# Optimization experiments

Measured on AMD Instinct MI355X. Metric: run time of the kernel, lower is better.

The kernel has to match this reference:

```python
import jax, jax.numpy as jnp
import numpy as np

GROUPS = 32
EPS = 1e-5


def setup_inputs() -> dict:
    key = jax.random.key(0)
    ks = jax.random.split(key, 8)
    B, C, H, W = 4, 512, 64, 64
    s = 1.0 / np.sqrt(C)  # conv1x1 fan-in init scale
    return {
        "x": jax.random.normal(ks[0], (B, C, H, W), dtype=jnp.float32),
        "gn_gamma": jnp.ones((C,), dtype=jnp.float32),
        "gn_beta": jnp.zeros((C,), dtype=jnp.float32),
        "wq": jax.random.normal(ks[1], (C, C), dtype=jnp.float32) * s,
        "bq": jnp.zeros((C,), dtype=jnp.float32),
        "wk": jax.random.normal(ks[2], (C, C), dtype=jnp.float32) * s,
        "bk": jnp.zeros((C,), dtype=jnp.float32),
        "wv": jax.random.normal(ks[3], (C, C), dtype=jnp.float32) * s,
        "bv": jnp.zeros((C,), dtype=jnp.float32),
    }


def reference(x, gn_gamma, gn_beta, wq, bq, wk, bk, wv, bv):
    B, C, H, W = x.shape
    N = H * W
    # GroupNorm over (channels-within-group, H, W)
    xg = x.reshape(B, GROUPS, C // GROUPS, H, W)
    mean = xg.mean(axis=(2, 3, 4), keepdims=True)
    var = xg.var(axis=(2, 3, 4), keepdims=True)
    xn = ((xg - mean) * jax.lax.rsqrt(var + EPS)).reshape(B, C, H, W)
    xn = xn * gn_gamma[None, :, None, None] + gn_beta[None, :, None, None]
    # 1x1 convs as channel matmuls over flattened spatial tokens: (B, C, N)
    xf = xn.reshape(B, C, N)
    q = jnp.einsum("oc,bcn->bon", wq, xf) + bq[None, :, None]  # (B, Co, N)
    k = jnp.einsum("oc,bcn->bon", wk, xf) + bk[None, :, None]
    v = jnp.einsum("oc,bcn->bon", wv, xf) + bv[None, :, None]
    # scores[b, m, n] = <Q_m, K_n> / sqrt(Co); full N x N matrix as in original
    scale = 1.0 / jnp.sqrt(jnp.asarray(C, dtype=x.dtype))
    scores = jnp.einsum("bcm,bcn->bmn", q, k) * scale  # (B, N, N)
    prob = jax.nn.softmax(scores, axis=-1)
    # out[b, c, m] = sum_n prob[b, m, n] * v[b, c, n]
    attn = jnp.einsum("bmn,bcn->bcm", prob, v).reshape(B, C, H, W)
    return x + attn  # ResLine is Identity since ch_in == ch_out
```

## Files before the change

### kernel.cpp

```cpp
#include <hip/hip_runtime.h>
#include <cstdint>

typedef __attribute__((ext_vector_type(8))) short short8;
typedef __attribute__((ext_vector_type(4))) float floatx4;
typedef __attribute__((ext_vector_type(8))) int intx8;

__device__ __forceinline__ unsigned short f2bf(float f) {
  unsigned int u = __float_as_uint(f);
  u += 0x7fffu + ((u >> 16) & 1u);
  return (unsigned short)(u >> 16);
}

__global__ __launch_bounds__(256) void gn_partial_kernel(
    const float* __restrict__ x, float* __restrict__ gsums) {
  const int b = blockIdx.x >> 8;
  const int g = (blockIdx.x >> 3) & 31;
  const int e = blockIdx.x & 7;
  const long long off = ((long long)(b * 512 + g * 16)) * 4096;
  const float4* xp = (const float4*)(x + off) + e * 2048;
  float s = 0.f, ss = 0.f;
  for (int i = threadIdx.x; i < 2048; i += 256) {
    float4 v = xp[i];
    s  += v.x + v.y + v.z + v.w;
    ss += v.x * v.x + v.y * v.y + v.z * v.z + v.w * v.w;
  }
  for (int off2 = 32; off2; off2 >>= 1) { s += __shfl_down(s, off2); ss += __shfl_down(ss, off2); }
  __shared__ float sb[8];
  const int lane = threadIdx.x & 63, wave = threadIdx.x >> 6;
  if (lane == 0) { sb[wave] = s; sb[4 + wave] = ss; }
  __syncthreads();
  if (threadIdx.x == 0) {
    atomicAdd(gsums + (b * 32 + g) * 2,     sb[0] + sb[1] + sb[2] + sb[3]);
    atomicAdd(gsums + (b * 32 + g) * 2 + 1, sb[4] + sb[5] + sb[6] + sb[7]);
  }
}

__global__ __launch_bounds__(256) void gn_finalize_kernel(
    const float* __restrict__ gsums, const float* __restrict__ gamma,
    const float* __restrict__ beta, float* __restrict__ scale,
    float* __restrict__ shift) {
  const int i = blockIdx.x * 256 + threadIdx.x;
  const int b = i >> 9;
  const int c = i & 511;
  const int g = c >> 4;
  const float S  = gsums[(b * 32 + g) * 2];
  const float SS = gsums[(b * 32 + g) * 2 + 1];
  const float mean = S * (1.f / 65536.f);
  const float var  = SS * (1.f / 65536.f) - mean * mean;
  const float inv  = rsqrtf(var + 1e-5f);
  const float sc = gamma[c] * inv;
  scale[i] = sc;
  shift[i] = beta[c] - mean * sc;
}

__global__ __launch_bounds__(256) void wcvt_zero_kernel(
    const float* __restrict__ wq, const float* __restrict__ wk,
    const float* __restrict__ wv, unsigned short* __restrict__ w16,
    float* __restrict__ zp, int nzero) {
  const int gi = blockIdx.x * 256 + threadIdx.x;
  if (gi < 196608) {
    const int m = gi >> 16;
    const int i = gi & 65535;
    const float* src = (m == 0) ? wq : (m == 1) ? wk : wv;
    float4 v = *((const float4*)src + i);
    ushort4 o;
    o.x = f2bf(v.x); o.y = f2bf(v.y); o.z = f2bf(v.z); o.w = f2bf(v.w);
    *((ushort4*)(w16 + (long long)m * 262144) + i) = o;
  } else {
    const int zi = gi - 196608;
    if (zi < nzero) zp[zi] = 0.f;
  }
}

__global__ __launch_bounds__(256) void norm_transpose_kernel(
    const float* __restrict__ x, const float* __restrict__ scale,
    const float* __restrict__ shift, unsigned short* __restrict__ xnt) {
  const int b = blockIdx.z;
  const int n0 = blockIdx.x * 64;
  const int c0 = blockIdx.y * 64;
  const int t = threadIdx.x;
  __shared__ unsigned short tile[64][65];
  {
    const int cl = t >> 2;
    const int nc = (t & 3) * 16;
    const int c = c0 + cl;
    const float* xp = x + ((long long)b * 512 + c) * 4096 + n0 + nc;
    const float sc = scale[b * 512 + c];
    const float sh = shift[b * 512 + c];
#pragma unroll
    for (int j = 0; j < 16; j += 4) {
      float4 v = *(const float4*)(xp + j);
      tile[cl][nc + j + 0] = f2bf(v.x * sc + sh);
      tile[cl][nc + j + 1] = f2bf(v.y * sc + sh);
      tile[cl][nc + j + 2] = f2bf(v.z * sc + sh);
      tile[cl][nc + j + 3] = f2bf(v.w * sc + sh);
    }
  }
  __syncthreads();
  {
    const int nl = t >> 2;
    const int cc = (t & 3) * 16;
    union { unsigned short u[16]; uint4 q[2]; } o;
#pragma unroll
    for (int j = 0; j < 16; ++j) o.u[j] = tile[cc + j][nl];
    unsigned short* op = xnt + ((long long)b * 4096 + n0 + nl) * 512 + c0 + cc;
    *((uint4*)op) = o.q[0];
    *((uint4*)op + 1) = o.q[1];
  }
}

__global__ __launch_bounds__(256) void zero_kernel(float* __restrict__ p, int n) {
  const int i = blockIdx.x * 256 + threadIdx.x;
  if (i < n) p[i] = 0.f;
}

template <int EPI>
__global__ __launch_bounds__(256) void gemm_tn_kernel(
    const unsigned short* __restrict__ A, const unsigned short* __restrict__ B,
    void* __restrict__ C, const float* __restrict__ bias,
    const float* __restrict__ bias2,
    int lda, int ldb, int ldc, int K,
    long long sA, long long sB, long long sC) {
  const int tid = threadIdx.x;
  const int lane = tid & 63;
  const int wave = tid >> 6;
  const int m0 = blockIdx.x * 128;
  const int n0 = blockIdx.y * 128;
  const int bz = blockIdx.z;
  A += (long long)bz * sA;
  B += (long long)bz * sB;

  __shared__ unsigned short smem[17408];
  unsigned short* As = smem;
  unsigned short* Bs = smem + 8192;

  floatx4 acc[4][4];
#pragma unroll
  for (int i = 0; i < 4; ++i)
#pragma unroll
    for (int j = 0; j < 4; ++j) acc[i][j] = (floatx4){0.f, 0.f, 0.f, 0.f};

  const unsigned short* ag[4];
  const unsigned short* bg[4];
  unsigned ldsoff[4];
#pragma unroll
  for (int i = 0; i < 4; ++i) {
    const int idx = i * 256 + tid;
    const int r = idx >> 3;
    const int g = idx & 7;
    const int gs = g ^ (r & 7);
    ag[i] = A + (long long)(m0 + r) * lda + gs * 8;
    bg[i] = B + (long long)(n0 + r) * ldb + gs * 8;
    ldsoff[i] = (unsigned)(i * 256 + wave * 64) * 8;
  }

  const int l15 = lane & 15;
  const int wm = (wave >> 1) * 64;
  const int wn = (wave & 1) * 64;

  for (int k0 = 0; k0 < K; k0 += 64) {
#pragma unroll
    for (int i = 0; i < 4; ++i) {
      __builtin_amdgcn_global_load_lds(
          (const __attribute__((address_space(1))) void*)(ag[i] + k0),
          (__attribute__((address_space(3))) void*)(As + ldsoff[i]), 16, 0, 0);
      __builtin_amdgcn_global_load_lds(
          (const __attribute__((address_space(1))) void*)(bg[i] + k0),
          (__attribute__((address_space(3))) void*)(Bs + ldsoff[i]), 16, 0, 0);
    }
    __syncthreads();
#pragma unroll
    for (int kk = 0; kk < 64; kk += 32) {
      const int gq = (kk >> 3) + (lane >> 4);
      short8 af[4], bfr[4];
#pragma unroll
      for (int mt = 0; mt < 4; ++mt) {
        const int row = wm + mt * 16 + l15;
        af[mt] = *(const short8*)&As[row * 64 + ((gq ^ (row & 7)) << 3)];
      }
#pragma unroll
      for (int nt = 0; nt < 4; ++nt) {
        const int row = wn + nt * 16 + l15;
        bfr[nt] = *(const short8*)&Bs[row * 64 + ((gq ^ (row & 7)) << 3)];
      }
#pragma unroll
      for (int mt = 0; mt < 4; ++mt)
#pragma unroll
        for (int nt = 0; nt < 4; ++nt)
          acc[mt][nt] = __builtin_amdgcn_mfma_f32_16x16x32_bf16(
              af[mt], bfr[nt], acc[mt][nt], 0, 0, 0);
    }
    __syncthreads();
  }

  const int r0 = (lane >> 4) * 4;

  if (EPI == 6) {
    unsigned char* t8 = (unsigned char*)smem;
    const float* bp = (m0 >= 512) ? bias2 : bias;
    const int mb = m0 & 511;
#pragma unroll
    for (int mt = 0; mt < 4; ++mt) {
      const int ml = wm + mt * 16 + r0;
      const float b0 = bp[mb + ml], b1 = bp[mb + ml + 1];
      const float b2 = bp[mb + ml + 2], b3 = bp[mb + ml + 3];
      const int gw = ml >> 4;
      const int mby = ml & 15;
#pragma unroll
      for (int nt = 0; nt < 4; ++nt) {
        const int nl = wn + nt * 16 + l15;
        int p = __builtin_amdgcn_cvt_pk_fp8_f32(acc[mt][nt][0] + b0,
                                                acc[mt][nt][1] + b1, 0, false);
        p = __builtin_amdgcn_cvt_pk_fp8_f32(acc[mt][nt][2] + b2,
                                            acc[mt][nt][3] + b3, p, true);
        *(int*)&t8[nl * 128 + ((gw ^ (nl & 7)) << 4) + mby] = p;
      }
    }
    __syncthreads();
    unsigned char* o8 = (unsigned char*)C + (long long)bz * sC;
#pragma unroll
    for (int t = 0; t < 4; ++t) {
      const int gid = t * 256 + tid;
      const int row = gid >> 3;
      const int gc = gid & 7;
      uint4 v = *(const uint4*)&t8[row * 128 + ((gc ^ (row & 7)) << 4)];
      *(uint4*)&o8[(long long)(n0 + row) * ldc + m0 + gc * 16] = v;
    }
    return;
  }

  if (EPI == 3) {
    unsigned char* t8 = (unsigned char*)smem;
#pragma unroll
    for (int mt = 0; mt < 4; ++mt) {
      const int ml = wm + mt * 16 + r0;
      const float b0 = bias[m0 + ml],     b1 = bias[m0 + ml + 1];
      const float b2 = bias[m0 + ml + 2], b3 = bias[m0 + ml + 3];
#pragma unroll
      for (int nt = 0; nt < 4; ++nt) {
        const int nl = wn + nt * 16 + l15;
        int p0 = __builtin_amdgcn_cvt_pk_fp8_f32(acc[mt][nt][0] + b0,
                                                 acc[mt][nt][1] + b1, 0, false);
        int p1 = __builtin_amdgcn_cvt_pk_fp8_f32(acc[mt][nt][2] + b2,
                                                 acc[mt][nt][3] + b3, 0, false);
        t8[(ml + 0) * 144 + nl] = (unsigned char)(p0 & 0xff);
        t8[(ml + 1) * 144 + nl] = (unsigned char)((p0 >> 8) & 0xff);
        t8[(ml + 2) * 144 + nl] = (unsigned char)(p1 & 0xff);
        t8[(ml + 3) * 144 + nl] = (unsigned char)((p1 >> 8) & 0xff);
      }
    }
    __syncthreads();
    unsigned char* o8 = (unsigned char*)C + (long long)bz * sC;
#pragma unroll
    for (int t = 0; t < 4; ++t) {
      const int gid = t * 256 + tid;
      const int row = gid >> 3;
      const int gc = gid & 7;
      uint4 v = *(const uint4*)&t8[row * 144 + gc * 16];
      *(uint4*)&o8[(long long)(m0 + row) * ldc + n0 + gc * 16] = v;
    }
    return;
  }

#pragma unroll
  for (int mt = 0; mt < 4; ++mt) {
#pragma unroll
    for (int nt = 0; nt < 4; ++nt) {
      const int nl = wn + nt * 16 + l15;
#pragma unroll
      for (int r = 0; r < 4; ++r) {
        const int ml = wm + mt * 16 + r0 + r;
        smem[ml * 136 + nl] = f2bf(acc[mt][nt][r] + bias[m0 + ml]);
      }
    }
  }
  __syncthreads();
  {
    unsigned short* o = (unsigned short*)C + (long long)bz * sC;
#pragma unroll
    for (int j = 0; j < 8; ++j) {
      const int gid = j * 256 + tid;
      const int m = gid >> 4;
      const int gc = gid & 15;
      short8 v = *(const short8*)&smem[m * 136 + gc * 8];
      *(short8*)&o[(long long)(m0 + m) * ldc + n0 + gc * 8] = v;
    }
  }
}

__global__ __launch_bounds__(256) void sgemm_fp8_kernel(
    const unsigned char* __restrict__ A, const unsigned char* __restrict__ B,
    unsigned char* __restrict__ S, float* __restrict__ lsum,
    long long sA, long long sB, long long sC, long long sL) {
  const int tid = threadIdx.x;
  const int lane = tid & 63;
  const int wave = tid >> 6;
  const int quad = lane >> 4;
  const int l15 = lane & 15;
  const int j0 = blockIdx.x * 128;
  const int i0 = blockIdx.y * 128;
  const int bz = blockIdx.z;
  A += (long long)bz * sA;
  B += (long long)bz * sB;

  __shared__ unsigned short smem[17408];
  unsigned char* As = (unsigned char*)smem;
  unsigned char* Bs = (unsigned char*)smem + 16384;

  floatx4 acc[4][4];
#pragma unroll
  for (int i = 0; i < 4; ++i)
#pragma unroll
    for (int j = 0; j < 4; ++j) acc[i][j] = (floatx4){0.f, 0.f, 0.f, 0.f};

  const unsigned char* ag[4];
  const unsigned char* bg[4];
  unsigned ldsoff[4];
#pragma unroll
  for (int i = 0; i < 4; ++i) {
    const int idx = i * 256 + tid;
    const int r = idx >> 3;
    const int g = idx & 7;
    const int gs = g ^ (r & 7);
    ag[i] = A + (long long)(j0 + r) * 1024 + gs * 16;
    bg[i] = B + (long long)(i0 + r) * 1024 + gs * 16;
    ldsoff[i] = (unsigned)(i * 256 + wave * 64) * 16;
  }

  const int wj = (wave >> 1) * 64;
  const int wi = (wave & 1) * 64;

  for (int k0 = 0; k0 < 512; k0 += 128) {
#pragma unroll
    for (int i = 0; i < 4; ++i) {
      __builtin_amdgcn_global_load_lds(
          (const __attribute__((address_space(1))) void*)(ag[i] + k0),
          (__attribute__((address_space(3))) void*)(As + ldsoff[i]), 16, 0, 0);
      __builtin_amdgcn_global_load_lds(
          (const __attribute__((address_space(1))) void*)(bg[i] + k0),
          (__attribute__((address_space(3))) void*)(Bs + ldsoff[i]), 16, 0, 0);
    }
    __syncthreads();
    intx8 af[4], bq[4];
#pragma unroll
    for (int t = 0; t < 4; ++t) {
      {
        const int row = wj + t * 16 + l15;
        const int r7 = row & 7;
        const uint4 x0 = *(const uint4*)(As + row * 128 + (((2 * quad) ^ r7) << 4));
        const uint4 x1 = *(const uint4*)(As + row * 128 + (((2 * quad + 1) ^ r7) << 4));
        af[t] = (intx8){(int)x0.x, (int)x0.y, (int)x0.z, (int)x0.w,
                        (int)x1.x, (int)x1.y, (int)x1.z, (int)x1.w};
      }
      {
        const int row = wi + t * 16 + l15;
        const int r7 = row & 7;
        const uint4 x0 = *(const uint4*)(Bs + row * 128 + (((2 * quad) ^ r7) << 4));
        const uint4 x1 = *(const uint4*)(Bs + row * 128 + (((2 * quad + 1) ^ r7) << 4));
        bq[t] = (intx8){(int)x0.x, (int)x0.y, (int)x0.z, (int)x0.w,
                        (int)x1.x, (int)x1.y, (int)x1.z, (int)x1.w};
      }
    }
#pragma unroll
    for (int jt = 0; jt < 4; ++jt)
#pragma unroll
      for (int it = 0; it < 4; ++it)
        acc[jt][it] = __builtin_amdgcn_mfma_scale_f32_16x16x128_f8f6f4(
            af[jt], bq[it], acc[jt][it], 0, 0, 0, 127, 0, 127);
    __syncthreads();
  }

  const float SCL = 0.044194173824159216f;
  const int jr = quad * 4;
  unsigned char* t8 = (unsigned char*)smem;
  float rs_it[4] = {0.f, 0.f, 0.f, 0.f};
#pragma unroll
  for (int jt = 0; jt < 4; ++jt) {
#pragma unroll
    for (int it = 0; it < 4; ++it) {
      const int il = wi + it * 16 + l15;
      const int jl = wj + jt * 16 + jr;
      const float e0 = __expf(acc[jt][it][0] * SCL);
      const float e1 = __expf(acc[jt][it][1] * SCL);
      const float e2 = __expf(acc[jt][it][2] * SCL);
      const float e3 = __expf(acc[jt][it][3] * SCL);
      rs_it[it] += e0 + e1 + e2 + e3;
      int p = __builtin_amdgcn_cvt_pk_fp8_f32(e0, e1, 0, false);
      p = __builtin_amdgcn_cvt_pk_fp8_f32(e2, e3, p, true);
      *(int*)&t8[il * 144 + jl] = p;
    }
  }
  float* lrow = lsum + (long long)bz * sL;
#pragma unroll
  for (int it = 0; it < 4; ++it) {
    float rs = rs_it[it];
    rs += __shfl_xor(rs, 16);
    rs += __shfl_xor(rs, 32);
    if (quad == 0) atomicAdd(lrow + i0 + wi + it * 16 + l15, rs);
  }
  __syncthreads();
  unsigned char* o = S + (long long)bz * sC;
#pragma unroll
  for (int t = 0; t < 4; ++t) {
    const int gid = t * 256 + tid;
    const int row = gid >> 3;
    const int gc = gid & 7;
    uint4 v = *(const uint4*)&t8[row * 144 + gc * 16];
    *(uint4*)&o[(long long)(i0 + row) * 4096 + j0 + gc * 16] = v;
  }
}

__global__ __launch_bounds__(512, 2) void pv_kernel(
    const unsigned char* __restrict__ A,
    const unsigned char* __restrict__ B,
    float* __restrict__ out, const float* __restrict__ res,
    const float* __restrict__ lsum,
    long long sA, long long sB, long long sC, long long sL) {
  const int id = blockIdx.x;
  const int xcd = id & 7;
  const int slot = id >> 3;
  const int m0 = (slot & 3) * 128;
  const int grp = xcd + 8 * (slot >> 2);
  const int n0 = (grp & 15) * 256;
  const int bz = grp >> 4;
  A += (long long)bz * sA;
  B += (long long)bz * sB;

  const int tid = threadIdx.x;
  const int lane = tid & 63;
  const int wave = tid >> 6;
  const int l15 = lane & 15;
  const int quad = lane >> 4;
  const int wm = (wave >> 2) * 64;
  const int wn = (wave & 3) * 64;

  __shared__ unsigned char smem[147456];

  floatx4 acc[4][4];
#pragma unroll
  for (int i = 0; i < 4; ++i)
#pragma unroll
    for (int j = 0; j < 4; ++j) acc[i][j] = (floatx4){0.f, 0.f, 0.f, 0.f};

  const unsigned char* ag[2];
  const unsigned char* bg[4];
  unsigned ao[2], bo[4];
#pragma unroll
  for (int j = 0; j < 2; ++j) {
    const int idx = j * 512 + tid;
    const int r = idx >> 3;
    const int g = idx & 7;
    ag[j] = A + (long long)(m0 + r) * 4096 + ((g ^ (r & 7)) << 4);
    ao[j] = (unsigned)(j * 512 + wave * 64) * 16;
  }
#pragma unroll
  for (int j = 0; j < 4; ++j) {
    const int idx = j * 512 + tid;
    const int r = idx >> 3;
    const int g = idx & 7;
    bg[j] = B + (long long)(n0 + r) * 4096 + ((g ^ (r & 7)) << 4);
    bo[j] = 16384u + (unsigned)(j * 512 + wave * 64) * 16;
  }

#define PV_GLDS(gp, lp)                                              \
  __builtin_amdgcn_global_load_lds(                                  \
      (const __attribute__((address_space(1))) void*)(gp),           \
      (__attribute__((address_space(3))) void*)(lp), 16, 0, 0)
#define PV_STAGE(tt, base)                                           \
  {                                                                  \
    PV_GLDS(ag[0] + (tt) * 128, smem + (base) + ao[0]);              \
    PV_GLDS(ag[1] + (tt) * 128, smem + (base) + ao[1]);              \
    PV_GLDS(bg[0] + (tt) * 128, smem + (base) + bo[0]);              \
    PV_GLDS(bg[1] + (tt) * 128, smem + (base) + bo[1]);              \
    PV_GLDS(bg[2] + (tt) * 128, smem + (base) + bo[2]);              \
    PV_GLDS(bg[3] + (tt) * 128, smem + (base) + bo[3]);              \
  }

  PV_STAGE(0, 0);
  PV_STAGE(1, 49152);
  asm volatile("s_waitcnt vmcnt(6)" ::: "memory");
  __builtin_amdgcn_s_barrier();

  int cur = 0;
  for (int t = 0; t < 32; ++t) {
    const unsigned char* As = smem + cur * 49152;
    const unsigned char* Bs = As + 16384;
    const int nb = (cur == 0) ? 2 : cur - 1;
    const int nbase = nb * 49152;
    const bool st = (t < 30);

    intx8 af[4], bq[4];
#pragma unroll
    for (int tt = 0; tt < 4; ++tt) {
      {
        const int row = wm + tt * 16 + l15;
        const int r7 = row & 7;
        const uint4 x0 = *(const uint4*)(As + row * 128 + (((2 * quad) ^ r7) << 4));
        const uint4 x1 = *(const uint4*)(As + row * 128 + (((2 * quad + 1) ^ r7) << 4));
        af[tt] = (intx8){(int)x0.x, (int)x0.y, (int)x0.z, (int)x0.w,
                         (int)x1.x, (int)x1.y, (int)x1.z, (int)x1.w};
      }
      {
        const int row = wn + tt * 16 + l15;
        const int r7 = row & 7;
        const uint4 x0 = *(const uint4*)(Bs + row * 128 + (((2 * quad) ^ r7) << 4));
        const uint4 x1 = *(const uint4*)(Bs + row * 128 + (((2 * quad + 1) ^ r7) << 4));
        bq[tt] = (intx8){(int)x0.x, (int)x0.y, (int)x0.z, (int)x0.w,
                         (int)x1.x, (int)x1.y, (int)x1.z, (int)x1.w};
      }
    }
    __builtin_amdgcn_sched_barrier(0);
    if (st) PV_STAGE(t + 2, nbase);
    asm volatile("s_waitcnt lgkmcnt(0)" ::: "memory");
    __builtin_amdgcn_sched_barrier(0);
    __builtin_amdgcn_s_setprio(1);
#pragma unroll
    for (int mt = 0; mt < 4; ++mt)
#pragma unroll
      for (int nt = 0; nt < 4; ++nt)
        acc[mt][nt] = __builtin_amdgcn_mfma_scale_f32_16x16x128_f8f6f4(
            af[mt], bq[nt], acc[mt][nt], 0, 0, 0, 127, 0, 127);
    __builtin_amdgcn_s_setprio(0);
    if (st) {
      asm volatile("s_waitcnt vmcnt(6)" ::: "memory");
    } else {
      asm volatile("s_waitcnt vmcnt(0)" ::: "memory");
    }
    __builtin_amdgcn_s_barrier();

    cur = (cur == 2) ? 0 : cur + 1;
  }
#undef PV_GLDS
#undef PV_STAGE

  const int r0 = (lane >> 4) * 4;
  float* o = out + (long long)bz * sC;
  const float* rr = res + (long long)bz * sC;
  const float* lrow = lsum + (long long)bz * sL;
  float inv[4];
#pragma unroll
  for (int nt = 0; nt < 4; ++nt) inv[nt] = 1.f / lrow[n0 + wn + nt * 16 + l15];
#pragma unroll
  for (int mt = 0; mt < 4; ++mt) {
#pragma unroll
    for (int nt = 0; nt < 4; ++nt) {
      const int n = n0 + wn + nt * 16 + l15;
#pragma unroll
      for (int r = 0; r < 4; ++r) {
        const int m = m0 + wm + mt * 16 + r0 + r;
        const long long off = (long long)m * 4096 + n;
        o[off] = acc[mt][nt][r] * inv[nt] + rr[off];
      }
    }
  }
}

extern "C" void kernel_launch(void* const* d_in, const int* in_sizes, int n_in,
                              void* d_out, int out_size, void* d_ws, size_t ws_size,
                              hipStream_t stream) {
  const float* x     = (const float*)d_in[0];
  const float* gamma = (const float*)d_in[1];
  const float* beta  = (const float*)d_in[2];
  const float* wq    = (const float*)d_in[3];
  const float* bq    = (const float*)d_in[4];
  const float* wk    = (const float*)d_in[5];
  const float* bk    = (const float*)d_in[6];
  const float* wv    = (const float*)d_in[7];
  const float* bv    = (const float*)d_in[8];
  float* out = (float*)d_out;

  const long long sTok = 4096LL * 512;
  const long long sQK8 = 4096LL * 1024;
  const long long sS8  = 4096LL * 4096;
  const long long sV8  = 512LL * 4096;

  char* ws = (char*)d_ws;
  float* scale = (float*)ws;
  float* shift = (float*)(ws + 8192);
  unsigned short* w16 = (unsigned short*)(ws + 16384);
  unsigned short* xnt = (unsigned short*)(ws + 1589248);
  unsigned char*  qk8 = (unsigned char*)(ws + 18366464);
  unsigned char*  vv8 = (unsigned char*)(ws + 51920896);

  const bool full = ws_size >= 202982400ULL;

  float* lsum;
  int nzero;
  if (full) {
    lsum = (float*)(ws + 202915840);
    nzero = 16384 + 256;
  } else {
    lsum = (float*)(ws + 102252544);
    nzero = 4096 + 256;
  }
  float* gsums = lsum + nzero - 256;

  wcvt_zero_kernel<<<768 + (nzero + 255) / 256, 256, 0, stream>>>(
      wq, wk, wv, w16, lsum, nzero);
  gn_partial_kernel<<<1024, 256, 0, stream>>>(x, gsums);
  gn_finalize_kernel<<<8, 256, 0, stream>>>(gsums, gamma, beta, scale, shift);
  norm_transpose_kernel<<<dim3(64, 8, 4), 256, 0, stream>>>(x, scale, shift, xnt);

  gemm_tn_kernel<6><<<dim3(8, 32, 4), 256, 0, stream>>>(
      w16, xnt, qk8, bq, bk, 512, 512, 1024, 512, 0, sTok, sQK8);
  gemm_tn_kernel<3><<<dim3(4, 32, 4), 256, 0, stream>>>(
      w16 + 524288, xnt, vv8, bv, nullptr, 512, 512, 4096, 512, 0, sTok, sV8);

  if (full) {
    unsigned char* S8 = (unsigned char*)(ws + 68698112);
    sgemm_fp8_kernel<<<dim3(32, 32, 4), 256, 0, stream>>>(
        qk8 + 512, qk8, S8, lsum, sQK8, sQK8, sS8, 4096);
    pv_kernel<<<256, 512, 0, stream>>>(
        vv8, S8, out, x, lsum, sV8, sS8, sTok, 4096);
  } else {
    unsigned char* S8 = (unsigned char*)(ws + 68698112);
    for (int b = 0; b < 4; ++b) {
      if (b) zero_kernel<<<16, 256, 0, stream>>>(lsum, 4096);
      sgemm_fp8_kernel<<<dim3(32, 32, 1), 256, 0, stream>>>(
          qk8 + (long long)b * sQK8 + 512, qk8 + (long long)b * sQK8, S8, lsum,
          0, 0, 0, 0);
      pv_kernel<<<64, 512, 0, stream>>>(
          vv8 + (long long)b * sV8, S8, out + (long long)b * sTok,
          x + (long long)b * sTok, lsum, 0, 0, 0, 0);
    }
  }
}
```

Before: 242.9 us.

## Enlarge QK score tile and triple-buffer fp8 loads into LDS

The fp8 score GEMM now uses 512-thread blocks computing 128x256 tiles, with eight waves in a 2x4 layout. Staging is three-deep: two stages are prefetched up front, and each iteration issues the next async global-to-LDS load before its MFMAs. Explicit vmcnt/lgkmcnt waits and raw barriers replace the two __syncthreads per K step, and MFMA issue is raised in priority. The goal is to hide global load latency and reuse each A tile across more columns. The cost is 144 KB of LDS per block, which limits occupancy to one block per CU.

New measurement: 246.5 us. No clear change (+1.5%).

```diff
diff --git a/kernel.cpp b/kernel.cpp
--- a/kernel.cpp
+++ b/kernel.cpp
@@ -288,24 +288,26 @@
   }
 }
 
-__global__ __launch_bounds__(256) void sgemm_fp8_kernel(
-    const unsigned char* __restrict__ A, const unsigned char* __restrict__ B,
+__global__ __launch_bounds__(512, 2) void sgemm_fp8_kernel(
+    const unsigned char* __restrict__ A,
+    const unsigned char* __restrict__ B,
     unsigned char* __restrict__ S, float* __restrict__ lsum,
     long long sA, long long sB, long long sC, long long sL) {
+  const int j0 = blockIdx.x * 128;
+  const int i0 = blockIdx.y * 256;
+  const int bz = blockIdx.z;
+  A += (long long)bz * sA;
+  B += (long long)bz * sB;
+
   const int tid = threadIdx.x;
   const int lane = tid & 63;
   const int wave = tid >> 6;
+  const int l15 = lane & 15;
   const int quad = lane >> 4;
-  const int l15 = lane & 15;
-  const int j0 = blockIdx.x * 128;
-  const int i0 = blockIdx.y * 128;
-  const int bz = blockIdx.z;
-  A += (long long)bz * sA;
-  B += (long long)bz * sB;
-
-  __shared__ unsigned short smem[17408];
-  unsigned char* As = (unsigned char*)smem;
-  unsigned char* Bs = (unsigned char*)smem + 16384;
+  const int wm = (wave >> 2) * 64;
+  const int wn = (wave & 3) * 64;
+
+  __shared__ unsigned char smem[147456];
 
   floatx4 acc[4][4];
 #pragma unroll
@@ -313,78 +315,111 @@
 #pragma unroll
     for (int j = 0; j < 4; ++j) acc[i][j] = (floatx4){0.f, 0.f, 0.f, 0.f};
 
-  const unsigned char* ag[4];
+  const unsigned char* ag[2];
   const unsigned char* bg[4];
-  unsigned ldsoff[4];
-#pragma unroll
-  for (int i = 0; i < 4; ++i) {
-    const int idx = i * 256 + tid;
+  unsigned ao[2], bo[4];
+#pragma unroll
+  for (int j = 0; j < 2; ++j) {
+    const int idx = j * 512 + tid;
     const int r = idx >> 3;
     const int g = idx & 7;
-    const int gs = g ^ (r & 7);
-    ag[i] = A + (long long)(j0 + r) * 1024 + gs * 16;
-    bg[i] = B + (long long)(i0 + r) * 1024 + gs * 16;
-    ldsoff[i] = (unsigned)(i * 256 + wave * 64) * 16;
-  }
-
-  const int wj = (wave >> 1) * 64;
-  const int wi = (wave & 1) * 64;
-
-  for (int k0 = 0; k0 < 512; k0 += 128) {
-#pragma unroll
-    for (int i = 0; i < 4; ++i) {
-      __builtin_amdgcn_global_load_lds(
-          (const __attribute__((address_space(1))) void*)(ag[i] + k0),
-          (__attribute__((address_space(3))) void*)(As + ldsoff[i]), 16, 0, 0);
-      __builtin_amdgcn_global_load_lds(
-          (const __attribute__((address_space(1))) void*)(bg[i] + k0),
-          (__attribute__((address_space(3))) void*)(Bs + ldsoff[i]), 16, 0, 0);
-    }
-    __syncthreads();
+    ag[j] = A + (long long)(j0 + r) * 1024 + ((g ^ (r & 7)) << 4);
+    ao[j] = (unsigned)(j * 512 + wave * 64) * 16;
+  }
+#pragma unroll
+  for (int j = 0; j < 4; ++j) {
+    const int idx = j * 512 + tid;
+    const int r = idx >> 3;
+    const int g = idx & 7;
+    bg[j] = B + (long long)(i0 + r) * 1024 + ((g ^ (r & 7)) << 4);
+    bo[j] = 16384u + (unsigned)(j * 512 + wave * 64) * 16;
+  }
+
+#define SG_GLDS(gp, lp)                                              \
+  __builtin_amdgcn_global_load_lds(                                  \
+      (const __attribute__((address_space(1))) void*)(gp),           \
+      (__attribute__((address_space(3))) void*)(lp), 16, 0, 0)
+#define SG_STAGE(tt, base)                                           \
+  {                                                                  \
+    SG_GLDS(ag[0] + (tt) * 128, smem + (base) + ao[0]);              \
+    SG_GLDS(ag[1] + (tt) * 128, smem + (base) + ao[1]);              \
+    SG_GLDS(bg[0] + (tt) * 128, smem + (base) + bo[0]);              \
+    SG_GLDS(bg[1] + (tt) * 128, smem + (base) + bo[1]);              \
+    SG_GLDS(bg[2] + (tt) * 128, smem + (base) + bo[2]);              \
+    SG_GLDS(bg[3] + (tt) * 128, smem + (base) + bo[3]);              \
+  }
+
+  SG_STAGE(0, 0);
+  SG_STAGE(1, 49152);
+  asm volatile("s_waitcnt vmcnt(6)" ::: "memory");
+  __builtin_amdgcn_s_barrier();
+
+  int cur = 0;
+  for (int t = 0; t < 4; ++t) {
+    const unsigned char* As = smem + cur * 49152;
+    const unsigned char* Bs = As + 16384;
+    const int nb = (cur == 0) ? 2 : cur - 1;
+    const int nbase = nb * 49152;
+    const bool st = (t < 2);
+
     intx8 af[4], bq[4];
 #pragma unroll
-    for (int t = 0; t < 4; ++t) {
+    for (int tt = 0; tt < 4; ++tt) {
       {
-        const int row = wj + t * 16 + l15;
+        const int row = wm + tt * 16 + l15;
         const int r7 = row & 7;
         const uint4 x0 = *(const uint4*)(As + row * 128 + (((2 * quad) ^ r7) << 4));
         const uint4 x1 = *(const uint4*)(As + row * 128 + (((2 * quad + 1) ^ r7) << 4));
-        af[t] = (intx8){(int)x0.x, (int)x0.y, (int)x0.z, (int)x0.w,
-                        (int)x1.x, (int)x1.y, (int)x1.z, (int)x1.w};
+        af[tt] = (intx8){(int)x0.x, (int)x0.y, (int)x0.z, (int)x0.w,
+                         (int)x1.x, (int)x1.y, (int)x1.z, (int)x1.w};
       }
       {
-        const int row = wi + t * 16 + l15;
+        const int row = wn + tt * 16 + l15;
         const int r7 = row & 7;
         const uint4 x0 = *(const uint4*)(Bs + row * 128 + (((2 * quad) ^ r7) << 4));
         const uint4 x1 = *(const uint4*)(Bs + row * 128 + (((2 * quad + 1) ^ r7) << 4));
-        bq[t] = (intx8){(int)x0.x, (int)x0.y, (int)x0.z, (int)x0.w,
-                        (int)x1.x, (int)x1.y, (int)x1.z, (int)x1.w};
-      }
-    }
-#pragma unroll
-    for (int jt = 0; jt < 4; ++jt)
-#pragma unroll
-      for (int it = 0; it < 4; ++it)
-        acc[jt][it] = __builtin_amdgcn_mfma_scale_f32_16x16x128_f8f6f4(
-            af[jt], bq[it], acc[jt][it], 0, 0, 0, 127, 0, 127);
-    __syncthreads();
-  }
+        bq[tt] = (intx8){(int)x0.x, (int)x0.y, (int)x0.z, (int)x0.w,
+                         (int)x1.x, (int)x1.y, (int)x1.z, (int)x1.w};
+      }
+    }
+    __builtin_amdgcn_sched_barrier(0);
+    if (st) SG_STAGE(t + 2, nbase);
+    asm volatile("s_waitcnt lgkmcnt(0)" ::: "memory");
+    __builtin_amdgcn_sched_barrier(0);
+    __builtin_amdgcn_s_setprio(1);
+#pragma unroll
+    for (int mt = 0; mt < 4; ++mt)
+#pragma unroll
+      for (int nt = 0; nt < 4; ++nt)
+        acc[mt][nt] = __builtin_amdgcn_mfma_scale_f32_16x16x128_f8f6f4(
+            af[mt], bq[nt], acc[mt][nt], 0, 0, 0, 127, 0, 127);
+    __builtin_amdgcn_s_setprio(0);
+    if (st) {
+      asm volatile("s_waitcnt vmcnt(6)" ::: "memory");
+    } else {
+      asm volatile("s_waitcnt vmcnt(0)" ::: "memory");
+    }
+    __builtin_amdgcn_s_barrier();
+
+    cur = (cur == 2) ? 0 : cur + 1;
+  }
+#undef SG_GLDS
+#undef SG_STAGE
 
   const float SCL = 0.044194173824159216f;
-  const int jr = quad * 4;
   unsigned char* t8 = (unsigned char*)smem;
-  float rs_it[4] = {0.f, 0.f, 0.f, 0.f};
-#pragma unroll
-  for (int jt = 0; jt < 4; ++jt) {
-#pragma unroll
-    for (int it = 0; it < 4; ++it) {
-      const int il = wi + it * 16 + l15;
-      const int jl = wj + jt * 16 + jr;
-      const float e0 = __expf(acc[jt][it][0] * SCL);
-      const float e1 = __expf(acc[jt][it][1] * SCL);
-      const float e2 = __expf(acc[jt][it][2] * SCL);
-      const float e3 = __expf(acc[jt][it][3] * SCL);
-      rs_it[it] += e0 + e1 + e2 + e3;
+  float rs_nt[4] = {0.f, 0.f, 0.f, 0.f};
+#pragma unroll
+  for (int mt = 0; mt < 4; ++mt) {
+#pragma unroll
+    for (int nt = 0; nt < 4; ++nt) {
+      const int il = wn + nt * 16 + l15;
+      const int jl = wm + mt * 16 + quad * 4;
+      const float e0 = __expf(acc[mt][nt][0] * SCL);
+      const float e1 = __expf(acc[mt][nt][1] * SCL);
+      const float e2 = __expf(acc[mt][nt][2] * SCL);
+      const float e3 = __expf(acc[mt][nt][3] * SCL);
+      rs_nt[nt] += e0 + e1 + e2 + e3;
       int p = __builtin_amdgcn_cvt_pk_fp8_f32(e0, e1, 0, false);
       p = __builtin_amdgcn_cvt_pk_fp8_f32(e2, e3, p, true);
       *(int*)&t8[il * 144 + jl] = p;
@@ -392,17 +427,17 @@
   }
   float* lrow = lsum + (long long)bz * sL;
 #pragma unroll
-  for (int it = 0; it < 4; ++it) {
-    float rs = rs_it[it];
+  for (int nt = 0; nt < 4; ++nt) {
+    float rs = rs_nt[nt];
     rs += __shfl_xor(rs, 16);
     rs += __shfl_xor(rs, 32);
-    if (quad == 0) atomicAdd(lrow + i0 + wi + it * 16 + l15, rs);
+    if (quad == 0) atomicAdd(lrow + i0 + wn + nt * 16 + l15, rs);
   }
   __syncthreads();
   unsigned char* o = S + (long long)bz * sC;
 #pragma unroll
   for (int t = 0; t < 4; ++t) {
-    const int gid = t * 256 + tid;
+    const int gid = t * 512 + tid;
     const int row = gid >> 3;
     const int gc = gid & 7;
     uint4 v = *(const uint4*)&t8[row * 144 + gc * 16];
@@ -608,7 +643,7 @@
 
   if (full) {
     unsigned char* S8 = (unsigned char*)(ws + 68698112);
-    sgemm_fp8_kernel<<<dim3(32, 32, 4), 256, 0, stream>>>(
+    sgemm_fp8_kernel<<<dim3(32, 16, 4), 512, 0, stream>>>(
         qk8 + 512, qk8, S8, lsum, sQK8, sQK8, sS8, 4096);
     pv_kernel<<<256, 512, 0, stream>>>(
         vv8, S8, out, x, lsum, sV8, sS8, sTok, 4096);
@@ -616,7 +651,7 @@
     unsigned char* S8 = (unsigned char*)(ws + 68698112);
     for (int b = 0; b < 4; ++b) {
       if (b) zero_kernel<<<16, 256, 0, stream>>>(lsum, 4096);
-      sgemm_fp8_kernel<<<dim3(32, 32, 1), 256, 0, stream>>>(
+      sgemm_fp8_kernel<<<dim3(32, 16, 1), 512, 0, stream>>>(
           qk8 + (long long)b * sQK8 + 512, qk8 + (long long)b * sQK8, S8, lsum,
           0, 0, 0, 0);
       pv_kernel<<<64, 512, 0, stream>>>(
```

## Fuse QK^T, softmax and PV into single flash-style attention kernel

Applied to the files above, without the earlier changes.

Replaces the separate fp8 score GEMM, which wrote a full 4096x4096 fp8 probability matrix per batch, and the PV kernel with one fused kernel. Each 512-thread block handles 64 query tokens. It streams K tiles through LDS, computes exp(scores) in registers and stages them briefly in LDS, then accumulates PV with V fragments loaded straight from global memory. Row sums are reduced in LDS, so the atomics, the lsum zeroing and the large score buffer all go away. The trade-offs are one block per CU with a simple single-buffered K prefetch, and exp is still taken without max subtraction.

Result: slower. 287.7 us (+18.4%).

```diff
diff --git a/kernel.cpp b/kernel.cpp
--- a/kernel.cpp
+++ b/kernel.cpp
@@ -109,11 +109,6 @@
   }
 }
 
-__global__ __launch_bounds__(256) void zero_kernel(float* __restrict__ p, int n) {
-  const int i = blockIdx.x * 256 + threadIdx.x;
-  if (i < n) p[i] = 0.f;
-}
-
 template <int EPI>
 __global__ __launch_bounds__(256) void gemm_tn_kernel(
     const unsigned short* __restrict__ A, const unsigned short* __restrict__ B,
@@ -261,295 +256,201 @@
     }
     return;
   }
-
-#pragma unroll
-  for (int mt = 0; mt < 4; ++mt) {
-#pragma unroll
-    for (int nt = 0; nt < 4; ++nt) {
-      const int nl = wn + nt * 16 + l15;
-#pragma unroll
-      for (int r = 0; r < 4; ++r) {
-        const int ml = wm + mt * 16 + r0 + r;
-        smem[ml * 136 + nl] = f2bf(acc[mt][nt][r] + bias[m0 + ml]);
-      }
-    }
-  }
-  __syncthreads();
-  {
-    unsigned short* o = (unsigned short*)C + (long long)bz * sC;
-#pragma unroll
-    for (int j = 0; j < 8; ++j) {
-      const int gid = j * 256 + tid;
-      const int m = gid >> 4;
-      const int gc = gid & 15;
-      short8 v = *(const short8*)&smem[m * 136 + gc * 8];
-      *(short8*)&o[(long long)(m0 + m) * ldc + n0 + gc * 8] = v;
-    }
-  }
-}
-
-__global__ __launch_bounds__(256) void sgemm_fp8_kernel(
-    const unsigned char* __restrict__ A, const unsigned char* __restrict__ B,
-    unsigned char* __restrict__ S, float* __restrict__ lsum,
-    long long sA, long long sB, long long sC, long long sL) {
-  const int tid = threadIdx.x;
-  const int lane = tid & 63;
-  const int wave = tid >> 6;
-  const int quad = lane >> 4;
-  const int l15 = lane & 15;
-  const int j0 = blockIdx.x * 128;
-  const int i0 = blockIdx.y * 128;
-  const int bz = blockIdx.z;
-  A += (long long)bz * sA;
-  B += (long long)bz * sB;
-
-  __shared__ unsigned short smem[17408];
-  unsigned char* As = (unsigned char*)smem;
-  unsigned char* Bs = (unsigned char*)smem + 16384;
-
-  floatx4 acc[4][4];
-#pragma unroll
-  for (int i = 0; i < 4; ++i)
-#pragma unroll
-    for (int j = 0; j < 4; ++j) acc[i][j] = (floatx4){0.f, 0.f, 0.f, 0.f};
-
-  const unsigned char* ag[4];
-  const unsigned char* bg[4];
-  unsigned ldsoff[4];
-#pragma unroll
-  for (int i = 0; i < 4; ++i) {
-    const int idx = i * 256 + tid;
-    const int r = idx >> 3;
-    const int g = idx & 7;
-    const int gs = g ^ (r & 7);
-    ag[i] = A + (long long)(j0 + r) * 1024 + gs * 16;
-    bg[i] = B + (long long)(i0 + r) * 1024 + gs * 16;
-    ldsoff[i] = (unsigned)(i * 256 + wave * 64) * 16;
-  }
-
-  const int wj = (wave >> 1) * 64;
-  const int wi = (wave & 1) * 64;
-
-  for (int k0 = 0; k0 < 512; k0 += 128) {
-#pragma unroll
-    for (int i = 0; i < 4; ++i) {
-      __builtin_amdgcn_global_load_lds(
-          (const __attribute__((address_space(1))) void*)(ag[i] + k0),
-          (__attribute__((address_space(3))) void*)(As + ldsoff[i]), 16, 0, 0);
-      __builtin_amdgcn_global_load_lds(
-          (const __attribute__((address_space(1))) void*)(bg[i] + k0),
-          (__attribute__((address_space(3))) void*)(Bs + ldsoff[i]), 16, 0, 0);
-    }
-    __syncthreads();
-    intx8 af[4], bq[4];
-#pragma unroll
-    for (int t = 0; t < 4; ++t) {
-      {
-        const int row = wj + t * 16 + l15;
-        const int r7 = row & 7;
-        const uint4 x0 = *(const uint4*)(As + row * 128 + (((2 * quad) ^ r7) << 4));
-        const uint4 x1 = *(const uint4*)(As + row * 128 + (((2 * quad + 1) ^ r7) << 4));
-        af[t] = (intx8){(int)x0.x, (int)x0.y, (int)x0.z, (int)x0.w,
-                        (int)x1.x, (int)x1.y, (int)x1.z, (int)x1.w};
-      }
-      {
-        const int row = wi + t * 16 + l15;
-        const int r7 = row & 7;
-        const uint4 x0 = *(const uint4*)(Bs + row * 128 + (((2 * quad) ^ r7) << 4));
-        const uint4 x1 = *(const uint4*)(Bs + row * 128 + (((2 * quad + 1) ^ r7) << 4));
-        bq[t] = (intx8){(int)x0.x, (int)x0.y, (int)x0.z, (int)x0.w,
-                        (int)x1.x, (int)x1.y, (int)x1.z, (int)x1.w};
-      }
-    }
-#pragma unroll
-    for (int jt = 0; jt < 4; ++jt)
-#pragma unroll
-      for (int it = 0; it < 4; ++it)
-        acc[jt][it] = __builtin_amdgcn_mfma_scale_f32_16x16x128_f8f6f4(
-            af[jt], bq[it], acc[jt][it], 0, 0, 0, 127, 0, 127);
-    __syncthreads();
-  }
-
-  const float SCL = 0.044194173824159216f;
-  const int jr = quad * 4;
-  unsigned char* t8 = (unsigned char*)smem;
-  float rs_it[4] = {0.f, 0.f, 0.f, 0.f};
-#pragma unroll
-  for (int jt = 0; jt < 4; ++jt) {
-#pragma unroll
-    for (int it = 0; it < 4; ++it) {
-      const int il = wi + it * 16 + l15;
-      const int jl = wj + jt * 16 + jr;
-      const float e0 = __expf(acc[jt][it][0] * SCL);
-      const float e1 = __expf(acc[jt][it][1] * SCL);
-      const float e2 = __expf(acc[jt][it][2] * SCL);
-      const float e3 = __expf(acc[jt][it][3] * SCL);
-      rs_it[it] += e0 + e1 + e2 + e3;
-      int p = __builtin_amdgcn_cvt_pk_fp8_f32(e0, e1, 0, false);
-      p = __builtin_amdgcn_cvt_pk_fp8_f32(e2, e3, p, true);
-      *(int*)&t8[il * 144 + jl] = p;
-    }
-  }
-  float* lrow = lsum + (long long)bz * sL;
-#pragma unroll
-  for (int it = 0; it < 4; ++it) {
-    float rs = rs_it[it];
-    rs += __shfl_xor(rs, 16);
-    rs += __shfl_xor(rs, 32);
-    if (quad == 0) atomicAdd(lrow + i0 + wi + it * 16 + l15, rs);
-  }
-  __syncthreads();
-  unsigned char* o = S + (long long)bz * sC;
-#pragma unroll
-  for (int t = 0; t < 4; ++t) {
-    const int gid = t * 256 + tid;
-    const int row = gid >> 3;
-    const int gc = gid & 7;
-    uint4 v = *(const uint4*)&t8[row * 144 + gc * 16];
-    *(uint4*)&o[(long long)(i0 + row) * 4096 + j0 + gc * 16] = v;
-  }
-}
-
-__global__ __launch_bounds__(512, 2) void pv_kernel(
-    const unsigned char* __restrict__ A,
-    const unsigned char* __restrict__ B,
-    float* __restrict__ out, const float* __restrict__ res,
-    const float* __restrict__ lsum,
-    long long sA, long long sB, long long sC, long long sL) {
+}
+
+__global__ __launch_bounds__(512, 1) void fused_attn_kernel(
+    const unsigned char* __restrict__ qk8,
+    const unsigned char* __restrict__ vv8,
+    float* __restrict__ out, const float* __restrict__ res) {
   const int id = blockIdx.x;
   const int xcd = id & 7;
   const int slot = id >> 3;
-  const int m0 = (slot & 3) * 128;
-  const int grp = xcd + 8 * (slot >> 2);
-  const int n0 = (grp & 15) * 256;
-  const int bz = grp >> 4;
-  A += (long long)bz * sA;
-  B += (long long)bz * sB;
+  const int bz = xcd & 3;
+  const int n0 = ((xcd >> 2) * 32 + slot) * 64;
+
+  const unsigned char* Q = qk8 + (long long)bz * (4096LL * 1024);
+  const unsigned char* K = Q + 512;
+  const unsigned char* V = vv8 + (long long)bz * (512LL * 4096);
 
   const int tid = threadIdx.x;
   const int lane = tid & 63;
   const int wave = tid >> 6;
   const int l15 = lane & 15;
   const int quad = lane >> 4;
-  const int wm = (wave >> 2) * 64;
-  const int wn = (wave & 3) * 64;
-
-  __shared__ unsigned char smem[147456];
+
+  __shared__ unsigned char smem[109568];
+  unsigned char* Qs = smem;
+  unsigned char* Ks = smem + 32768;
+  unsigned char* Ps = smem + 98304;
+  float* red = (float*)(smem + 107520);
 
   floatx4 acc[4][4];
 #pragma unroll
   for (int i = 0; i < 4; ++i)
 #pragma unroll
     for (int j = 0; j < 4; ++j) acc[i][j] = (floatx4){0.f, 0.f, 0.f, 0.f};
-
-  const unsigned char* ag[2];
-  const unsigned char* bg[4];
-  unsigned ao[2], bo[4];
-#pragma unroll
-  for (int j = 0; j < 2; ++j) {
-    const int idx = j * 512 + tid;
-    const int r = idx >> 3;
-    const int g = idx & 7;
-    ag[j] = A + (long long)(m0 + r) * 4096 + ((g ^ (r & 7)) << 4);
-    ao[j] = (unsigned)(j * 512 + wave * 64) * 16;
-  }
-#pragma unroll
-  for (int j = 0; j < 4; ++j) {
-    const int idx = j * 512 + tid;
-    const int r = idx >> 3;
-    const int g = idx & 7;
-    bg[j] = B + (long long)(n0 + r) * 4096 + ((g ^ (r & 7)) << 4);
-    bo[j] = 16384u + (unsigned)(j * 512 + wave * 64) * 16;
-  }
-
-#define PV_GLDS(gp, lp)                                              \
+  float rs[4] = {0.f, 0.f, 0.f, 0.f};
+
+#define FA_GLDS(gp, lp)                                              \
   __builtin_amdgcn_global_load_lds(                                  \
       (const __attribute__((address_space(1))) void*)(gp),           \
       (__attribute__((address_space(3))) void*)(lp), 16, 0, 0)
-#define PV_STAGE(tt, base)                                           \
-  {                                                                  \
-    PV_GLDS(ag[0] + (tt) * 128, smem + (base) + ao[0]);              \
-    PV_GLDS(ag[1] + (tt) * 128, smem + (base) + ao[1]);              \
-    PV_GLDS(bg[0] + (tt) * 128, smem + (base) + bo[0]);              \
-    PV_GLDS(bg[1] + (tt) * 128, smem + (base) + bo[1]);              \
-    PV_GLDS(bg[2] + (tt) * 128, smem + (base) + bo[2]);              \
-    PV_GLDS(bg[3] + (tt) * 128, smem + (base) + bo[3]);              \
-  }
-
-  PV_STAGE(0, 0);
-  PV_STAGE(1, 49152);
-  asm volatile("s_waitcnt vmcnt(6)" ::: "memory");
-  __builtin_amdgcn_s_barrier();
-
-  int cur = 0;
+
+  const unsigned char* kg[8];
+  unsigned ko[8];
+#pragma unroll
+  for (int j = 0; j < 8; ++j) {
+    const int idx = j * 512 + tid;
+    const int r = idx >> 5;
+    const int g = idx & 31;
+    const int gs = (g & 24) | ((g & 7) ^ (r & 7));
+    kg[j] = K + (long long)r * 1024 + gs * 16;
+    ko[j] = 32768u + (unsigned)(j * 512 + wave * 64) * 16;
+  }
+  {
+#pragma unroll
+    for (int j = 0; j < 4; ++j) {
+      const int idx = j * 512 + tid;
+      const int r = idx >> 5;
+      const int g = idx & 31;
+      const int gs = (g & 24) | ((g & 7) ^ (r & 7));
+      FA_GLDS(Q + (long long)(n0 + r) * 1024 + gs * 16,
+              smem + (unsigned)(j * 512 + wave * 64) * 16);
+    }
+#pragma unroll
+    for (int j = 0; j < 8; ++j) FA_GLDS(kg[j], smem + ko[j]);
+    asm volatile("s_waitcnt vmcnt(0)" ::: "memory");
+    __builtin_amdgcn_s_barrier();
+  }
+
+  const unsigned char* vg[4];
+#pragma unroll
+  for (int cs = 0; cs < 4; ++cs)
+    vg[cs] = V + (long long)(wave * 64 + cs * 16 + l15) * 4096 + quad * 32;
+
+  const float SCL = 0.044194173824159216f;
+
   for (int t = 0; t < 32; ++t) {
-    const unsigned char* As = smem + cur * 49152;
-    const unsigned char* Bs = As + 16384;
-    const int nb = (cur == 0) ? 2 : cur - 1;
-    const int nbase = nb * 49152;
-    const bool st = (t < 30);
-
-    intx8 af[4], bq[4];
-#pragma unroll
-    for (int tt = 0; tt < 4; ++tt) {
+    const int jcol = t * 128;
+
+    uint4 vf[4][2];
+#pragma unroll
+    for (int cs = 0; cs < 4; ++cs) {
+      vf[cs][0] = *(const uint4*)(vg[cs] + jcol);
+      vf[cs][1] = *(const uint4*)(vg[cs] + jcol + 16);
+    }
+    __builtin_amdgcn_sched_barrier(0);
+
+    floatx4 sacc[4];
+#pragma unroll
+    for (int ns = 0; ns < 4; ++ns) sacc[ns] = (floatx4){0.f, 0.f, 0.f, 0.f};
+#pragma unroll
+    for (int kc = 0; kc < 4; ++kc) {
+      intx8 af;
       {
-        const int row = wm + tt * 16 + l15;
+        const int row = wave * 16 + l15;
         const int r7 = row & 7;
-        const uint4 x0 = *(const uint4*)(As + row * 128 + (((2 * quad) ^ r7) << 4));
-        const uint4 x1 = *(const uint4*)(As + row * 128 + (((2 * quad + 1) ^ r7) << 4));
-        af[tt] = (intx8){(int)x0.x, (int)x0.y, (int)x0.z, (int)x0.w,
-                         (int)x1.x, (int)x1.y, (int)x1.z, (int)x1.w};
-      }
-      {
-        const int row = wn + tt * 16 + l15;
+        const uint4 x0 = *(const uint4*)(Ks + row * 512 + kc * 128 +
+                                         (((2 * quad) ^ r7) << 4));
+        const uint4 x1 = *(const uint4*)(Ks + row * 512 + kc * 128 +
+                                         (((2 * quad + 1) ^ r7) << 4));
+        af = (intx8){(int)x0.x, (int)x0.y, (int)x0.z, (int)x0.w,
+                     (int)x1.x, (int)x1.y, (int)x1.z, (int)x1.w};
+      }
+#pragma unroll
+      for (int ns = 0; ns < 4; ++ns) {
+        const int row = ns * 16 + l15;
         const int r7 = row & 7;
-        const uint4 x0 = *(const uint4*)(Bs + row * 128 + (((2 * quad) ^ r7) << 4));
-        const uint4 x1 = *(const uint4*)(Bs + row * 128 + (((2 * quad + 1) ^ r7) << 4));
-        bq[tt] = (intx8){(int)x0.x, (int)x0.y, (int)x0.z, (int)x0.w,
-                         (int)x1.x, (int)x1.y, (int)x1.z, (int)x1.w};
-      }
-    }
-    __builtin_amdgcn_sched_barrier(0);
-    if (st) PV_STAGE(t + 2, nbase);
+        const uint4 x0 = *(const uint4*)(Qs + row * 512 + kc * 128 +
+                                         (((2 * quad) ^ r7) << 4));
+        const uint4 x1 = *(const uint4*)(Qs + row * 512 + kc * 128 +
+                                         (((2 * quad + 1) ^ r7) << 4));
+        const intx8 bq = (intx8){(int)x0.x, (int)x0.y, (int)x0.z, (int)x0.w,
+                                 (int)x1.x, (int)x1.y, (int)x1.z, (int)x1.w};
+        sacc[ns] = __builtin_amdgcn_mfma_scale_f32_16x16x128_f8f6f4(
+            af, bq, sacc[ns], 0, 0, 0, 127, 0, 127);
+      }
+    }
+
+#pragma unroll
+    for (int ns = 0; ns < 4; ++ns) {
+      const float e0 = __expf(sacc[ns][0] * SCL);
+      const float e1 = __expf(sacc[ns][1] * SCL);
+      const float e2 = __expf(sacc[ns][2] * SCL);
+      const float e3 = __expf(sacc[ns][3] * SCL);
+      rs[ns] += e0 + e1 + e2 + e3;
+      int p = __builtin_amdgcn_cvt_pk_fp8_f32(e0, e1, 0, false);
+      p = __builtin_amdgcn_cvt_pk_fp8_f32(e2, e3, p, true);
+      *(int*)&Ps[(ns * 16 + l15) * 144 + wave * 16 + quad * 4] = p;
+    }
     asm volatile("s_waitcnt lgkmcnt(0)" ::: "memory");
     __builtin_amdgcn_sched_barrier(0);
+    __builtin_amdgcn_s_barrier();
+
+    if (t < 31) {
+      const long long koff = (long long)(t + 1) * 131072;
+#pragma unroll
+      for (int j = 0; j < 8; ++j) FA_GLDS(kg[j] + koff, smem + ko[j]);
+    }
+    __builtin_amdgcn_sched_barrier(0);
+
+    intx8 pb[4];
+#pragma unroll
+    for (int ns = 0; ns < 4; ++ns) {
+      const int row = ns * 16 + l15;
+      const uint4 x0 = *(const uint4*)(Ps + row * 144 + quad * 32);
+      const uint4 x1 = *(const uint4*)(Ps + row * 144 + quad * 32 + 16);
+      pb[ns] = (intx8){(int)x0.x, (int)x0.y, (int)x0.z, (int)x0.w,
+                       (int)x1.x, (int)x1.y, (int)x1.z, (int)x1.w};
+    }
     __builtin_amdgcn_s_setprio(1);
 #pragma unroll
-    for (int mt = 0; mt < 4; ++mt)
-#pragma unroll
-      for (int nt = 0; nt < 4; ++nt)
-        acc[mt][nt] = __builtin_amdgcn_mfma_scale_f32_16x16x128_f8f6f4(
-            af[mt], bq[nt], acc[mt][nt], 0, 0, 0, 127, 0, 127);
+    for (int cs = 0; cs < 4; ++cs) {
+      const intx8 av = (intx8){(int)vf[cs][0].x, (int)vf[cs][0].y,
+                               (int)vf[cs][0].z, (int)vf[cs][0].w,
+                               (int)vf[cs][1].x, (int)vf[cs][1].y,
+                               (int)vf[cs][1].z, (int)vf[cs][1].w};
+#pragma unroll
+      for (int ns = 0; ns < 4; ++ns)
+        acc[cs][ns] = __builtin_amdgcn_mfma_scale_f32_16x16x128_f8f6f4(
+            av, pb[ns], acc[cs][ns], 0, 0, 0, 127, 0, 127);
+    }
     __builtin_amdgcn_s_setprio(0);
-    if (st) {
-      asm volatile("s_waitcnt vmcnt(6)" ::: "memory");
-    } else {
-      asm volatile("s_waitcnt vmcnt(0)" ::: "memory");
-    }
+
+    asm volatile("s_waitcnt vmcnt(0)" ::: "memory");
     __builtin_amdgcn_s_barrier();
-
-    cur = (cur == 2) ? 0 : cur + 1;
-  }
-#undef PV_GLDS
-#undef PV_STAGE
-
-  const int r0 = (lane >> 4) * 4;
-  float* o = out + (long long)bz * sC;
-  const float* rr = res + (long long)bz * sC;
-  const float* lrow = lsum + (long long)bz * sL;
+  }
+#undef FA_GLDS
+
+#pragma unroll
+  for (int ns = 0; ns < 4; ++ns) {
+    float r = rs[ns];
+    r += __shfl_xor(r, 16);
+    r += __shfl_xor(r, 32);
+    if (quad == 0) red[wave * 64 + ns * 16 + l15] = r;
+  }
+  __syncthreads();
   float inv[4];
 #pragma unroll
-  for (int nt = 0; nt < 4; ++nt) inv[nt] = 1.f / lrow[n0 + wn + nt * 16 + l15];
-#pragma unroll
-  for (int mt = 0; mt < 4; ++mt) {
-#pragma unroll
-    for (int nt = 0; nt < 4; ++nt) {
-      const int n = n0 + wn + nt * 16 + l15;
+  for (int ns = 0; ns < 4; ++ns) {
+    float s = 0.f;
+#pragma unroll
+    for (int w = 0; w < 8; ++w) s += red[w * 64 + ns * 16 + l15];
+    inv[ns] = 1.f / s;
+  }
+
+  float* o = out + (long long)bz * (4096LL * 512);
+  const float* rr = res + (long long)bz * (4096LL * 512);
+#pragma unroll
+  for (int cs = 0; cs < 4; ++cs) {
+#pragma unroll
+    for (int ns = 0; ns < 4; ++ns) {
+      const int n = n0 + ns * 16 + l15;
 #pragma unroll
       for (int r = 0; r < 4; ++r) {
-        const int m = m0 + wm + mt * 16 + r0 + r;
-        const long long off = (long long)m * 4096 + n;
-        o[off] = acc[mt][nt][r] * inv[nt] + rr[off];
+        const int c = wave * 64 + cs * 16 + quad * 4 + r;
+        const long long off = (long long)c * 4096 + n;
+        o[off] = acc[cs][ns][r] * inv[ns] + rr[off];
       }
     }
   }
@@ -571,7 +472,6 @@
 
   const long long sTok = 4096LL * 512;
   const long long sQK8 = 4096LL * 1024;
-  const long long sS8  = 4096LL * 4096;
   const long long sV8  = 512LL * 4096;
 
   char* ws = (char*)d_ws;
@@ -581,22 +481,9 @@
   unsigned short* xnt = (unsigned short*)(ws + 1589248);
   unsigned char*  qk8 = (unsigned char*)(ws + 18366464);
   unsigned char*  vv8 = (unsigned char*)(ws + 51920896);
-
-  const bool full = ws_size >= 202982400ULL;
-
-  float* lsum;
-  int nzero;
-  if (full) {
-    lsum = (float*)(ws + 202915840);
-    nzero = 16384 + 256;
-  } else {
-    lsum = (float*)(ws + 102252544);
-    nzero = 4096 + 256;
-  }
-  float* gsums = lsum + nzero - 256;
-
-  wcvt_zero_kernel<<<768 + (nzero + 255) / 256, 256, 0, stream>>>(
-      wq, wk, wv, w16, lsum, nzero);
+  float* gsums = (float*)(ws + 60317696);
+
+  wcvt_zero_kernel<<<769, 256, 0, stream>>>(wq, wk, wv, w16, gsums, 256);
   gn_partial_kernel<<<1024, 256, 0, stream>>>(x, gsums);
   gn_finalize_kernel<<<8, 256, 0, stream>>>(gsums, gamma, beta, scale, shift);
   norm_transpose_kernel<<<dim3(64, 8, 4), 256, 0, stream>>>(x, scale, shift, xnt);
@@ -606,22 +493,5 @@
   gemm_tn_kernel<3><<<dim3(4, 32, 4), 256, 0, stream>>>(
       w16 + 524288, xnt, vv8, bv, nullptr, 512, 512, 4096, 512, 0, sTok, sV8);
 
-  if (full) {
-    unsigned char* S8 = (unsigned char*)(ws + 68698112);
-    sgemm_fp8_kernel<<<dim3(32, 32, 4), 256, 0, stream>>>(
-        qk8 + 512, qk8, S8, lsum, sQK8, sQK8, sS8, 4096);
-    pv_kernel<<<256, 512, 0, stream>>>(
-        vv8, S8, out, x, lsum, sV8, sS8, sTok, 4096);
-  } else {
-    unsigned char* S8 = (unsigned char*)(ws + 68698112);
-    for (int b = 0; b < 4; ++b) {
-      if (b) zero_kernel<<<16, 256, 0, stream>>>(lsum, 4096);
-      sgemm_fp8_kernel<<<dim3(32, 32, 1), 256, 0, stream>>>(
-          qk8 + (long long)b * sQK8 + 512, qk8 + (long long)b * sQK8, S8, lsum,
-          0, 0, 0, 0);
-      pv_kernel<<<64, 512, 0, stream>>>(
-          vv8 + (long long)b * sV8, S8, out + (long long)b * sTok,
-          x + (long long)b * sTok, lsum, 0, 0, 0, 0);
-    }
-  }
-}
+  fused_attn_kernel<<<256, 512, 0, stream>>>(qk8, vv8, out, x);
+}
```
